# Kernel optimization log

Hardware: AMD Instinct MI355X
Metric: run time of the kernel (lower is better)

## Reference

```python
import jax, jax.numpy as jnp
import numpy as np

B, N = 16, 64
EMB, CDIM, NL = 32, 24, 3      # emb_dim, cloud_dim, number of degrees l=0..2 (cloudord)
NBASIS, H, RADIUS = 10, 150, 2.0
BETA = 5.0                     # rescaled_act.Softplus(beta=5)


def sp(x):
    return jax.nn.softplus(BETA * x) / BETA


def cosine_basis(r):
    # CosineBasisModel: cos^2 bumps on centers linspace(0, max_radius, nbasis)
    centers = jnp.linspace(0.0, RADIUS, NBASIS).astype(r.dtype)
    step = RADIUS / (NBASIS - 1)
    d = (r[..., None] - centers) / step
    return jnp.where(jnp.abs(d) < 1.0, jnp.cos(0.5 * jnp.pi * d) ** 2, 0.0)


def sph_harm(u):
    # real spherical harmonics l=0,1,2 on unit vectors u[...,3]
    x, y, z = u[..., 0], u[..., 1], u[..., 2]
    Y0 = jnp.full(u.shape[:-1] + (1,), 0.28209479177387814, u.dtype)
    c1 = 0.4886025119029199
    Y1 = c1 * jnp.stack([y, z, x], -1)
    c2a, c2b, c2c = 1.0925484305920792, 0.31539156525252005, 0.5462742152960396
    Y2 = jnp.stack([c2a * x * y, c2a * y * z, c2b * (3 * z * z - 1.0),
                    c2a * x * z, c2c * (x * x - y * y)], -1)
    return [Y0, Y1, Y2]


def setup_inputs() -> dict:
    key = jax.random.key(0)
    ks = jax.random.split(key, 16)
    d = {}
    d['xyz'] = jax.random.normal(ks[0], (B, N, 3), jnp.float32)
    d['Z'] = jax.random.randint(ks[1], (B, N), 0, 6)
    d['body23'] = jax.random.normal(ks[2], (B, N, 3), jnp.float32)
    # embedding table (6 species)
    d['emb_W'] = jax.random.normal(ks[3], (6, EMB), jnp.float32) * 0.1
    # radial model MLP: NBASIS -> 150 -> 150 -> 150 -> NL*CDIM*EMB
    ROUT = NL * CDIM * EMB
    d['rW0'] = jax.random.normal(ks[4], (NBASIS, H), jnp.float32) / np.sqrt(NBASIS)
    d['rb0'] = jnp.zeros((H,), jnp.float32)
    d['rW1'] = jax.random.normal(ks[5], (H, H), jnp.float32) / np.sqrt(H)
    d['rb1'] = jnp.zeros((H,), jnp.float32)
    d['rW2'] = jax.random.normal(ks[6], (H, H), jnp.float32) / np.sqrt(H)
    d['rb2'] = jnp.zeros((H,), jnp.float32)
    d['rW3'] = jax.random.normal(ks[7], (H, ROUT), jnp.float32) / np.sqrt(H)
    d['rb3'] = jnp.zeros((ROUT,), jnp.float32)
    # AtomResiduals (1 block) on 219 channels
    CR = CDIM * NL * NL + 3  # 219
    d['res_W'] = jax.random.normal(ks[8], (CR, CR), jnp.float32) / np.sqrt(CR)
    d['res_b'] = jnp.zeros((CR,), jnp.float32)
    # collate: Linear(438,128) + BatchNorm1d(128)
    d['c_W'] = jax.random.normal(ks[9], (2 * CR, 128), jnp.float32) / np.sqrt(2 * CR)
    d['c_b'] = jnp.zeros((128,), jnp.float32)
    d['bn_g'] = jnp.ones((128,), jnp.float32)
    d['bn_b'] = jnp.zeros((128,), jnp.float32)
    # output layer
    d['o_W'] = jax.random.normal(ks[10], (128, 1), jnp.float32) / np.sqrt(128.0)
    d['o_b'] = jnp.zeros((1,), jnp.float32)
    return d


def reference(xyz, Z, body23, emb_W, rW0, rb0, rW1, rb1, rW2, rb2, rW3, rb3,
              res_W, res_b, c_W, c_b, bn_g, bn_b, o_W, o_b):
    f = emb_W[Z]                                        # [B,N,EMB] atom embeddings
    diff = xyz[:, :, None, :] - xyz[:, None, :, :]      # [B,N,N,3]
    r = jnp.sqrt(jnp.sum(diff * diff, -1) + 1e-12)      # [B,N,N]
    mask = ((r < RADIUS) & (r > 1e-6)).astype(f.dtype)  # neighbors within radius, no self
    u = diff / r[..., None]
    Ys = sph_harm(u)                                    # [ [B,N,N,1], [..,3], [..,5] ]
    # radial model on all pairs
    h = sp(cosine_basis(r) @ rW0 + rb0)
    h = sp(h @ rW1 + rb1)
    h = sp(h @ rW2 + rb2)
    R = (h @ rW3 + rb3).reshape(B, N, N, NL, CDIM, EMB)
    R = R * mask[..., None, None, None]
    # equivariant neighbor convolution: out[a,co,l,m] = sum_n,ci R_l(r_an) Y_lm(u_an) f[n,ci]
    outs = []
    for l in range(NL):
        o = jnp.einsum('banoi,banm,bni->baom', R[..., l, :, :], Ys[l], f)
        outs.append(o.reshape(B, N, -1) / jnp.sqrt(float(N)))
    feats = jnp.concatenate(outs, -1)                   # [B,N,216]
    feats = jnp.concatenate([body23, feats], -1)        # [B,N,219] (final_res concat)
    # AtomResiduals: concat(x, x + sp(Linear(x))) -> channel doubling
    res = feats + sp(feats @ res_W + res_b)
    feats = jnp.concatenate([feats, res], -1)           # [B,N,438]
    # lp_pool2d(norm_type=2, kernel=(N,1)): sqrt of sum of squares over atoms
    pooled = jnp.sqrt(jnp.sum(feats * feats, axis=1))   # [B,438]
    # collate: softplus(Linear), softplus(BatchNorm1d) (training-mode batch stats)
    hh = jax.nn.softplus(pooled @ c_W + c_b)
    mu = hh.mean(0)
    var = hh.var(0)
    hh = jax.nn.softplus((hh - mu) / jnp.sqrt(var + 1e-5) * bn_g + bn_b)
    return jax.nn.sigmoid(hh @ o_W + o_b)               # [B,1]
```

## Files before the change

kernel.cpp:

```cpp
#include <hip/hip_runtime.h>
#include <math.h>

constexpr int cB  = 16;
constexpr int cN  = 64;
constexpr int EMB = 32;
constexpr int NL  = 3;
constexpr int CDIM = 24;
constexpr int LOD = NL * CDIM;
constexpr int NB  = 10;
constexpr int H   = 150;
constexpr int CR  = 219;
constexpr int C2  = 438;
constexpr int HD  = 128;
constexpr int NSP = 6;
constexpr int GC  = NSP * LOD;
constexpr int GCP = 512;
constexpr int TBL = 512;
constexpr float RADIUS = 2.0f;

__device__ __forceinline__ float sp5(float x) {
    return fmaxf(x, 0.0f) + 0.2f * log1pf(expf(-5.0f * fabsf(x)));
}
__device__ __forceinline__ float sp1(float x) {
    return fmaxf(x, 0.0f) + log1pf(expf(-fabsf(x)));
}

__global__ void __launch_bounds__(256) k_prep(const float* __restrict__ emb_W,
                                              const float* __restrict__ rW3,
                                              const float* __restrict__ rb3,
                                              const float* __restrict__ rW0,
                                              const float* __restrict__ rW1,
                                              const float* __restrict__ rW2,
                                              const float* __restrict__ c_W,
                                              const float* __restrict__ res_W,
                                              float* __restrict__ W2,
                                              float* __restrict__ Pbz,
                                              float* __restrict__ rW0p,
                                              float* __restrict__ rW1p,
                                              float* __restrict__ rW2p,
                                              float* __restrict__ c_Wt,
                                              float* __restrict__ pooled2,
                                              float* __restrict__ touch) {
    int bx = blockIdx.x;
    int t = threadIdx.x;
    __shared__ float e[EMB];
    if (bx < 90) {
        int z = bx / 15, hb = bx - (bx / 15) * 15;
        if (t < EMB) e[t] = emb_W[z * EMB + t];
        __syncthreads();
        for (int o = t; o < 10 * LOD; o += 256) {
            int k = hb * 10 + o / LOD, lo = o % LOD;
            const float* wr = &rW3[(size_t)k * (LOD * EMB) + lo * EMB];
            float s = 0.0f;
            #pragma unroll
            for (int i = 0; i < EMB; ++i) s = fmaf(wr[i], e[i], s);
            W2[(size_t)k * GCP + z * LOD + lo] = s;
        }
        if (z == 0) {
            for (int o = t; o < 10 * (GCP - GC); o += 256) {
                int k = hb * 10 + o / (GCP - GC), c = GC + o % (GCP - GC);
                W2[(size_t)k * GCP + c] = 0.0f;
            }
        }
        if (hb == 0 && t < LOD) {
            float s = 0.0f;
            #pragma unroll
            for (int i = 0; i < EMB; ++i) s = fmaf(rb3[t * EMB + i], e[i], s);
            Pbz[z * LOD + t] = s;
        }
    } else if (bx < 346) {
        int pb = bx - 90;
        int total = NB * 152 + 2 * H * 152 + HD * 440;
        int total2 = total + cB * C2;
        for (int i = pb * 256 + t; i < total2; i += 256 * 256) {
            if (i < NB * 152) {
                int r = i / 152, c = i - r * 152;
                rW0p[i] = (c < H) ? rW0[r * H + c] : 0.0f;
            } else if (i < NB * 152 + H * 152) {
                int j = i - NB * 152; int r = j / 152, c = j - r * 152;
                rW1p[j] = (c < H) ? rW1[r * H + c] : 0.0f;
            } else if (i < NB * 152 + 2 * H * 152) {
                int j = i - NB * 152 - H * 152; int r = j / 152, c = j - r * 152;
                rW2p[j] = (c < H) ? rW2[r * H + c] : 0.0f;
            } else if (i < total) {
                int j = i - NB * 152 - 2 * H * 152;
                int jj = j / 440, ch = j - jj * 440;
                c_Wt[j] = (ch < C2) ? c_W[ch * HD + jj] : 0.0f;
            } else {
                pooled2[i - total] = 0.0f;
            }
        }
    } else {
        int wb = bx - 346;
        const int n4 = (CR * CR) / 4;
        float s = 0.0f;
        for (int i = wb * 256 + t; i < n4; i += 64 * 256) {
            float4 v = *(const float4*)&res_W[4 * i];
            s += v.x + v.y + v.z + v.w;
        }
        touch[wb * 256 + t] = s;
    }
}

__global__ void __launch_bounds__(256) k_chain(const float* __restrict__ rW0p,
                                               const float* __restrict__ rb0,
                                               const float* __restrict__ rW1p,
                                               const float* __restrict__ rb1,
                                               const float* __restrict__ rW2p,
                                               const float* __restrict__ rb2,
                                               const float* __restrict__ W2,
                                               const float* __restrict__ Pbz,
                                               float* __restrict__ G) {
    const int row0 = blockIdx.x * 2;
    const int t = threadIdx.x;
    const int a2 = t >> 7;
    const int jt = t & 127;
    const bool hasx = (jt < 22);
    const int jx = hasx ? 128 + jt : 128;

    __shared__ __align__(16) float bas[2][10];
    __shared__ __align__(16) float hA[2 * 152];
    __shared__ __align__(16) float hB[2 * 152];

    if (t < 2) {
        float r = (float)(row0 + t) * (RADIUS / (float)(TBL - 1));
        #pragma unroll
        for (int k = 0; k < NB; ++k) {
            float d = r * 4.5f - (float)k;
            float v = 0.0f;
            if (fabsf(d) < 1.0f) { float cc = cosf(1.57079632679489662f * d); v = cc * cc; }
            bas[t][k] = v;
        }
    }
    __syncthreads();

    {
        float a0 = 0, ax = 0;
        #pragma unroll
        for (int k = 0; k < NB; ++k) {
            float x = bas[a2][k];
            a0 = fmaf(x, rW0p[k * 152 + jt], a0);
            ax = fmaf(x, rW0p[k * 152 + jx], ax);
        }
        hA[a2 * 152 + jt] = sp5(a0 + rb0[jt]);
        if (hasx) hA[a2 * 152 + 128 + jt] = sp5(ax + rb0[128 + jt]);
    }
    __syncthreads();

    for (int layer = 0; layer < 2; ++layer) {
        const float* W   = layer ? rW2p : rW1p;
        const float* bb  = layer ? rb2 : rb1;
        const float* src = layer ? hB : hA;
        float*       dst = layer ? hA : hB;
        float a0 = 0, ax = 0;
        const float* xs = &src[a2 * 152];
        #pragma unroll 10
        for (int k = 0; k < H; ++k) {
            float x = xs[k];
            const float* wr = &W[k * 152];
            a0 = fmaf(x, wr[jt], a0);
            ax = fmaf(x, wr[jx], ax);
        }
        dst[a2 * 152 + jt] = sp5(a0 + bb[jt]);
        if (hasx) dst[a2 * 152 + 128 + jt] = sp5(ax + bb[128 + jt]);
        __syncthreads();
    }

    if (jt < 108) {
        const int g0 = 4 * jt;
        float4 c0 = {0, 0, 0, 0};
        const float* xs = &hA[a2 * 152];
        #pragma unroll 10
        for (int k = 0; k < H; ++k) {
            float x = xs[k];
            float4 w = *(const float4*)&W2[(size_t)k * GCP + g0];
            c0.x = fmaf(x, w.x, c0.x); c0.y = fmaf(x, w.y, c0.y);
            c0.z = fmaf(x, w.z, c0.z); c0.w = fmaf(x, w.w, c0.w);
        }
        int row = row0 + a2;
        float4 p = *(const float4*)&Pbz[g0];
        float4 o;
        o.x = c0.x + p.x; o.y = c0.y + p.y; o.z = c0.z + p.z; o.w = c0.w + p.w;
        *(float4*)&G[(size_t)row * GC + g0] = o;
    }
}

__global__ void __launch_bounds__(256) k_red(const float* __restrict__ xyz,
                                             const int* __restrict__ Z,
                                             const float* __restrict__ body23,
                                             const float* __restrict__ G,
                                             const float* __restrict__ res_W,
                                             const float* __restrict__ res_b,
                                             float* __restrict__ pooled2) {
    int ba = blockIdx.x;
    int b = ba >> 6, a = ba & 63;
    int t = threadIdx.x;
    __shared__ float ym[64][12];
    __shared__ float ymc[64][12];
    __shared__ __align__(16) float ps[64][76];
    __shared__ float xr[224];
    __shared__ int t0s[64];
    __shared__ float wls[64];
    __shared__ int zs[64];
    __shared__ int alist[64];
    __shared__ int cnt_s;
    if (t < 64) {
        int n = t;
        float ax = xyz[((size_t)b * cN + a) * 3 + 0];
        float ay = xyz[((size_t)b * cN + a) * 3 + 1];
        float az = xyz[((size_t)b * cN + a) * 3 + 2];
        float d0 = ax - xyz[((size_t)b * cN + n) * 3 + 0];
        float d1 = ay - xyz[((size_t)b * cN + n) * 3 + 1];
        float d2 = az - xyz[((size_t)b * cN + n) * 3 + 2];
        float s = d0 * d0 + d1 * d1 + d2 * d2;
        float r = sqrtf(s + 1e-12f);
        bool m = (r < RADIUS) && (r > 1e-6f);
        float u = r * ((float)(TBL - 1) / RADIUS);
        int t0 = (int)u;
        if (t0 > TBL - 2) t0 = TBL - 2;
        t0s[n] = t0;
        wls[n] = u - (float)t0;
        zs[n] = Z[b * cN + n];
        float inv = 1.0f / r;
        float x = d0 * inv, y = d1 * inv, z = d2 * inv;
        ym[n][0] = 0.28209479177387814f;
        ym[n][1] = 0.4886025119029199f * y;
        ym[n][2] = 0.4886025119029199f * z;
        ym[n][3] = 0.4886025119029199f * x;
        ym[n][4] = 1.0925484305920792f * x * y;
        ym[n][5] = 1.0925484305920792f * y * z;
        ym[n][6] = 0.31539156525252005f * (3.0f * z * z - 1.0f);
        ym[n][7] = 1.0925484305920792f * x * z;
        ym[n][8] = 0.5462742152960396f * (x * x - y * y);
        unsigned long long mask = __ballot(m);
        int rank = __popcll(mask & ((1ull << n) - 1ull));
        if (m) alist[rank] = n;
        if (n == 0) cnt_s = (int)__popcll(mask);
    }
    __syncthreads();
    int cnt = cnt_s;
    for (int i = t; i < cnt * 9; i += 256) {
        int ci = i / 9, yi = i - ci * 9;
        ymc[ci][yi] = ym[alist[ci]][yi];
    }
    for (int i = t; i < cnt * 18; i += 256) {
        int ci = i / 18, q = i - ci * 18;
        int n = alist[ci];
        const float* g = &G[(size_t)t0s[n] * GC + zs[n] * LOD + 4 * q];
        float4 g0 = *(const float4*)g;
        float4 g1 = *(const float4*)(g + GC);
        float wl = wls[n];
        float4 v;
        v.x = g0.x + wl * (g1.x - g0.x);
        v.y = g0.y + wl * (g1.y - g0.y);
        v.z = g0.z + wl * (g1.z - g0.z);
        v.w = g0.w + wl * (g1.w - g0.w);
        *(float4*)&ps[ci][4 * q] = v;
    }
    __syncthreads();
    if (t < 216) {
        int lo, yi;
        if (t < 24) { lo = t; yi = 0; }
        else if (t < 96) { int q = t - 24; int o = q / 3; lo = 24 + o; yi = 1 + (q - o * 3); }
        else { int q = t - 96; int o = q / 5; lo = 48 + o; yi = 4 + (q - o * 5); }
        float acc = 0.0f;
        #pragma unroll 4
        for (int ci = 0; ci < cnt; ++ci)
            acc = fmaf(ps[ci][lo], ymc[ci][yi], acc);
        xr[3 + t] = acc * 0.125f;
    } else if (t < 219) {
        xr[t - 216] = body23[(size_t)ba * 3 + (t - 216)];
    }
    __syncthreads();
    if (t < CR) {
        float xv = xr[t];
        float s = 0.0f;
        #pragma unroll 8
        for (int k = 0; k < CR; ++k)
            s = fmaf(xr[k], res_W[(size_t)k * CR + t], s);
        float o = xv + sp5(res_b[t] + s);
        atomicAdd(&pooled2[b * C2 + t],      xv * xv);
        atomicAdd(&pooled2[b * C2 + CR + t], o * o);
    }
}

__global__ void __launch_bounds__(64) k_head1(const float* __restrict__ pooled2,
                                              const float* __restrict__ c_Wt,
                                              const float* __restrict__ c_b,
                                              float* __restrict__ hh) {
    int j = blockIdx.x;
    int l = threadIdx.x;
    float acc[cB];
    #pragma unroll
    for (int b = 0; b < cB; ++b) acc[b] = 0.0f;
    const float* wr = &c_Wt[j * 440];
    for (int ch = l; ch < C2; ch += 64) {
        float wv = wr[ch];
        #pragma unroll
        for (int b = 0; b < cB; ++b)
            acc[b] = fmaf(sqrtf(pooled2[b * C2 + ch]), wv, acc[b]);
    }
    #pragma unroll
    for (int off = 32; off >= 1; off >>= 1) {
        #pragma unroll
        for (int b = 0; b < cB; ++b) acc[b] += __shfl_xor(acc[b], off, 64);
    }
    if (l == 0) {
        float cb = c_b[j];
        #pragma unroll
        for (int b = 0; b < cB; ++b) hh[b * HD + j] = sp1(acc[b] + cb);
    }
}

__global__ void __launch_bounds__(128) k_head2(const float* __restrict__ hh,
                                               const float* __restrict__ bn_g,
                                               const float* __restrict__ bn_b,
                                               const float* __restrict__ o_W,
                                               const float* __restrict__ o_b,
                                               float* __restrict__ out) {
    __shared__ float hh2[cB][HD];
    int t = threadIdx.x;
    float v[cB];
    float mu = 0.0f;
    #pragma unroll
    for (int b = 0; b < cB; ++b) { v[b] = hh[b * HD + t]; mu += v[b]; }
    mu *= (1.0f / cB);
    float var = 0.0f;
    #pragma unroll
    for (int b = 0; b < cB; ++b) { float d = v[b] - mu; var = fmaf(d, d, var); }
    var *= (1.0f / cB);
    float sc = bn_g[t] / sqrtf(var + 1e-5f);
    float bnb = bn_b[t];
    #pragma unroll
    for (int b = 0; b < cB; ++b) hh2[b][t] = sp1((v[b] - mu) * sc + bnb);
    __syncthreads();
    if (t < cB) {
        float s = o_b[0];
        for (int j = 0; j < HD; ++j) s = fmaf(hh2[t][j], o_W[j], s);
        out[t] = 1.0f / (1.0f + expf(-s));
    }
}

extern "C" void kernel_launch(void* const* d_in, const int* in_sizes, int n_in,
                              void* d_out, int out_size, void* d_ws, size_t ws_size,
                              hipStream_t stream) {
    const float* xyz    = (const float*)d_in[0];
    const int*   Z      = (const int*)d_in[1];
    const float* body23 = (const float*)d_in[2];
    const float* emb_W  = (const float*)d_in[3];
    const float* rW0    = (const float*)d_in[4];
    const float* rb0    = (const float*)d_in[5];
    const float* rW1    = (const float*)d_in[6];
    const float* rb1    = (const float*)d_in[7];
    const float* rW2    = (const float*)d_in[8];
    const float* rb2    = (const float*)d_in[9];
    const float* rW3    = (const float*)d_in[10];
    const float* rb3    = (const float*)d_in[11];
    const float* res_W  = (const float*)d_in[12];
    const float* res_b  = (const float*)d_in[13];
    const float* c_W    = (const float*)d_in[14];
    const float* c_b    = (const float*)d_in[15];
    const float* bn_g   = (const float*)d_in[16];
    const float* bn_b   = (const float*)d_in[17];
    const float* o_W    = (const float*)d_in[18];
    const float* o_b    = (const float*)d_in[19];

    float* w       = (float*)d_ws;
    float* W2      = w;
    float* Pbz     = W2 + 76800;
    float* rW0p    = Pbz + 432;
    float* rW1p    = rW0p + 1520;
    float* rW2p    = rW1p + 22800;
    float* c_Wt    = rW2p + 22800;
    float* G       = c_Wt + 56320;
    float* pooled2 = G + 221184;
    float* hh      = pooled2 + 7008;
    float* touch   = hh + 2048;
    (void)in_sizes; (void)n_in; (void)out_size; (void)ws_size;

    k_prep <<<410, 256, 0, stream>>>(emb_W, rW3, rb3, rW0, rW1, rW2, c_W, res_W,
                                     W2, Pbz, rW0p, rW1p, rW2p, c_Wt, pooled2, touch);
    k_chain<<<TBL / 2, 256, 0, stream>>>(rW0p, rb0, rW1p, rb1, rW2p, rb2, W2, Pbz, G);
    k_red  <<<cB * cN, 256, 0, stream>>>(xyz, Z, body23, G, res_W, res_b, pooled2);
    k_head1<<<HD, 64, 0, stream>>>(pooled2, c_Wt, c_b, hh);
    k_head2<<<1, 128, 0, stream>>>(hh, bn_g, bn_b, o_W, o_b, (float*)d_out);
}
```

Baseline: 66.66 us.

## Fuse batchnorm/output head into head1 via atomics and drop padded MLP weight copies

Removes the k_prep stage that copied rW0/rW1/rW2 into 152-column padded buffers; k_chain now reads the original row-major weights with stride H. The two head kernels are merged into one. Each block computes batch-norm statistics for its own channel, atomically adds its contribution to per-sample logits, and the last block, found with an atomic counter, applies the sigmoid. This saves one kernel launch and some prep traffic. The trade-off is float atomics, which make the summation order nondeterministic, plus unaligned weight row starts.

```diff
diff --git a/kernel.cpp b/kernel.cpp
--- a/kernel.cpp
+++ b/kernel.cpp
@@ -28,18 +28,13 @@
 __global__ void __launch_bounds__(256) k_prep(const float* __restrict__ emb_W,
                                               const float* __restrict__ rW3,
                                               const float* __restrict__ rb3,
-                                              const float* __restrict__ rW0,
-                                              const float* __restrict__ rW1,
-                                              const float* __restrict__ rW2,
                                               const float* __restrict__ c_W,
                                               const float* __restrict__ res_W,
                                               float* __restrict__ W2,
                                               float* __restrict__ Pbz,
-                                              float* __restrict__ rW0p,
-                                              float* __restrict__ rW1p,
-                                              float* __restrict__ rW2p,
                                               float* __restrict__ c_Wt,
                                               float* __restrict__ pooled2,
+                                              float* __restrict__ logit,
                                               float* __restrict__ touch) {
     int bx = blockIdx.x;
     int t = threadIdx.x;
@@ -68,30 +63,8 @@
             for (int i = 0; i < EMB; ++i) s = fmaf(rb3[t * EMB + i], e[i], s);
             Pbz[z * LOD + t] = s;
         }
-    } else if (bx < 346) {
-        int pb = bx - 90;
-        int total = NB * 152 + 2 * H * 152 + HD * 440;
-        int total2 = total + cB * C2;
-        for (int i = pb * 256 + t; i < total2; i += 256 * 256) {
-            if (i < NB * 152) {
-                int r = i / 152, c = i - r * 152;
-                rW0p[i] = (c < H) ? rW0[r * H + c] : 0.0f;
-            } else if (i < NB * 152 + H * 152) {
-                int j = i - NB * 152; int r = j / 152, c = j - r * 152;
-                rW1p[j] = (c < H) ? rW1[r * H + c] : 0.0f;
-            } else if (i < NB * 152 + 2 * H * 152) {
-                int j = i - NB * 152 - H * 152; int r = j / 152, c = j - r * 152;
-                rW2p[j] = (c < H) ? rW2[r * H + c] : 0.0f;
-            } else if (i < total) {
-                int j = i - NB * 152 - 2 * H * 152;
-                int jj = j / 440, ch = j - jj * 440;
-                c_Wt[j] = (ch < C2) ? c_W[ch * HD + jj] : 0.0f;
-            } else {
-                pooled2[i - total] = 0.0f;
-            }
-        }
-    } else {
-        int wb = bx - 346;
+    } else if (bx < 154) {
+        int wb = bx - 90;
         const int n4 = (CR * CR) / 4;
         float s = 0.0f;
         for (int i = wb * 256 + t; i < n4; i += 64 * 256) {
@@ -99,14 +72,28 @@
             s += v.x + v.y + v.z + v.w;
         }
         touch[wb * 256 + t] = s;
-    }
-}
-
-__global__ void __launch_bounds__(256) k_chain(const float* __restrict__ rW0p,
+    } else {
+        int pb = bx - 154;
+        int totalT = HD * 440;
+        int total2 = totalT + cB * C2 + 16 + 1;
+        for (int i = pb * 256 + t; i < total2; i += 32 * 256) {
+            if (i < totalT) {
+                int jj = i / 440, ch = i - jj * 440;
+                c_Wt[i] = (ch < C2) ? c_W[ch * HD + jj] : 0.0f;
+            } else if (i < totalT + cB * C2) {
+                pooled2[i - totalT] = 0.0f;
+            } else {
+                logit[i - totalT - cB * C2] = 0.0f;
+            }
+        }
+    }
+}
+
+__global__ void __launch_bounds__(256) k_chain(const float* __restrict__ rW0,
                                                const float* __restrict__ rb0,
-                                               const float* __restrict__ rW1p,
+                                               const float* __restrict__ rW1,
                                                const float* __restrict__ rb1,
-                                               const float* __restrict__ rW2p,
+                                               const float* __restrict__ rW2,
                                                const float* __restrict__ rb2,
                                                const float* __restrict__ W2,
                                                const float* __restrict__ Pbz,
@@ -139,8 +126,8 @@
         #pragma unroll
         for (int k = 0; k < NB; ++k) {
             float x = bas[a2][k];
-            a0 = fmaf(x, rW0p[k * 152 + jt], a0);
-            ax = fmaf(x, rW0p[k * 152 + jx], ax);
+            a0 = fmaf(x, rW0[k * H + jt], a0);
+            ax = fmaf(x, rW0[k * H + jx], ax);
         }
         hA[a2 * 152 + jt] = sp5(a0 + rb0[jt]);
         if (hasx) hA[a2 * 152 + 128 + jt] = sp5(ax + rb0[128 + jt]);
@@ -148,7 +135,7 @@
     __syncthreads();
 
     for (int layer = 0; layer < 2; ++layer) {
-        const float* W   = layer ? rW2p : rW1p;
+        const float* W   = layer ? rW2 : rW1;
         const float* bb  = layer ? rb2 : rb1;
         const float* src = layer ? hB : hA;
         float*       dst = layer ? hA : hB;
@@ -157,7 +144,7 @@
         #pragma unroll 10
         for (int k = 0; k < H; ++k) {
             float x = xs[k];
-            const float* wr = &W[k * 152];
+            const float* wr = &W[k * H];
             a0 = fmaf(x, wr[jt], a0);
             ax = fmaf(x, wr[jx], ax);
         }
@@ -284,10 +271,15 @@
     }
 }
 
-__global__ void __launch_bounds__(64) k_head1(const float* __restrict__ pooled2,
+__global__ void __launch_bounds__(64) k_headm(const float* __restrict__ pooled2,
                                               const float* __restrict__ c_Wt,
                                               const float* __restrict__ c_b,
-                                              float* __restrict__ hh) {
+                                              const float* __restrict__ bn_g,
+                                              const float* __restrict__ bn_b,
+                                              const float* __restrict__ o_W,
+                                              const float* __restrict__ o_b,
+                                              float* __restrict__ logit,
+                                              float* __restrict__ out) {
     int j = blockIdx.x;
     int l = threadIdx.x;
     float acc[cB];
@@ -305,39 +297,34 @@
         #pragma unroll
         for (int b = 0; b < cB; ++b) acc[b] += __shfl_xor(acc[b], off, 64);
     }
+    __shared__ int is_last;
     if (l == 0) {
         float cb = c_b[j];
-        #pragma unroll
-        for (int b = 0; b < cB; ++b) hh[b * HD + j] = sp1(acc[b] + cb);
-    }
-}
-
-__global__ void __launch_bounds__(128) k_head2(const float* __restrict__ hh,
-                                               const float* __restrict__ bn_g,
-                                               const float* __restrict__ bn_b,
-                                               const float* __restrict__ o_W,
-                                               const float* __restrict__ o_b,
-                                               float* __restrict__ out) {
-    __shared__ float hh2[cB][HD];
-    int t = threadIdx.x;
-    float v[cB];
-    float mu = 0.0f;
-    #pragma unroll
-    for (int b = 0; b < cB; ++b) { v[b] = hh[b * HD + t]; mu += v[b]; }
-    mu *= (1.0f / cB);
-    float var = 0.0f;
-    #pragma unroll
-    for (int b = 0; b < cB; ++b) { float d = v[b] - mu; var = fmaf(d, d, var); }
-    var *= (1.0f / cB);
-    float sc = bn_g[t] / sqrtf(var + 1e-5f);
-    float bnb = bn_b[t];
-    #pragma unroll
-    for (int b = 0; b < cB; ++b) hh2[b][t] = sp1((v[b] - mu) * sc + bnb);
-    __syncthreads();
-    if (t < cB) {
-        float s = o_b[0];
-        for (int j = 0; j < HD; ++j) s = fmaf(hh2[t][j], o_W[j], s);
-        out[t] = 1.0f / (1.0f + expf(-s));
+        float h[cB];
+        float mu = 0.0f;
+        #pragma unroll
+        for (int b = 0; b < cB; ++b) { h[b] = sp1(acc[b] + cb); mu += h[b]; }
+        mu *= (1.0f / cB);
+        float var = 0.0f;
+        #pragma unroll
+        for (int b = 0; b < cB; ++b) { float d = h[b] - mu; var = fmaf(d, d, var); }
+        var *= (1.0f / cB);
+        float sc = bn_g[j] / sqrtf(var + 1e-5f);
+        float bnb = bn_b[j];
+        float ow = o_W[j];
+        #pragma unroll
+        for (int b = 0; b < cB; ++b) {
+            float h2 = sp1((h[b] - mu) * sc + bnb);
+            atomicAdd(&logit[b], h2 * ow);
+        }
+        __threadfence();
+        unsigned int old = atomicAdd((unsigned int*)&logit[16], 1u);
+        is_last = (old == (unsigned int)(HD - 1));
+    }
+    __syncthreads();
+    if (is_last && l < cB) {
+        float s = atomicAdd(&logit[l], 0.0f) + o_b[0];
+        out[l] = 1.0f / (1.0f + expf(-s));
     }
 }
 
@@ -368,20 +355,17 @@
     float* w       = (float*)d_ws;
     float* W2      = w;
     float* Pbz     = W2 + 76800;
-    float* rW0p    = Pbz + 432;
-    float* rW1p    = rW0p + 1520;
-    float* rW2p    = rW1p + 22800;
-    float* c_Wt    = rW2p + 22800;
+    float* c_Wt    = Pbz + 432;
     float* G       = c_Wt + 56320;
     float* pooled2 = G + 221184;
-    float* hh      = pooled2 + 7008;
-    float* touch   = hh + 2048;
+    float* logit   = pooled2 + 7008;
+    float* touch   = logit + 32;
     (void)in_sizes; (void)n_in; (void)out_size; (void)ws_size;
 
-    k_prep <<<410, 256, 0, stream>>>(emb_W, rW3, rb3, rW0, rW1, rW2, c_W, res_W,
-                                     W2, Pbz, rW0p, rW1p, rW2p, c_Wt, pooled2, touch);
-    k_chain<<<TBL / 2, 256, 0, stream>>>(rW0p, rb0, rW1p, rb1, rW2p, rb2, W2, Pbz, G);
+    k_prep <<<186, 256, 0, stream>>>(emb_W, rW3, rb3, c_W, res_W,
+                                     W2, Pbz, c_Wt, pooled2, logit, touch);
+    k_chain<<<TBL / 2, 256, 0, stream>>>(rW0, rb0, rW1, rb1, rW2, rb2, W2, Pbz, G);
     k_red  <<<cB * cN, 256, 0, stream>>>(xyz, Z, body23, G, res_W, res_b, pooled2);
-    k_head1<<<HD, 64, 0, stream>>>(pooled2, c_Wt, c_b, hh);
-    k_head2<<<1, 128, 0, stream>>>(hh, bn_g, bn_b, o_W, o_b, (float*)d_out);
-}
+    k_headm<<<HD, 64, 0, stream>>>(pooled2, c_Wt, c_b, bn_g, bn_b, o_W, o_b,
+                                   logit, (float*)d_out);
+}
```

New measurement: 80.86 us. 21.3% more time.
